# Kernel tuning notes

Measured on AMD Instinct MI355X. Metric: run time of the kernel, lower is better.

## Reference

```python
import jax, jax.numpy as jnp
import numpy as np

N_NODES = 100000
N_EDGES = 1600000
D = 128
NUM_EXPERTS = 8
NUM_LAYERS = 2
EPS = 1e-5


def setup_inputs() -> dict:
    key = jax.random.key(0)
    ks = jax.random.split(key, 8)
    x = jax.random.normal(ks[0], (N_NODES, D), dtype=jnp.float32)
    edge_index = jax.random.randint(ks[1], (2, N_EDGES), 0, N_NODES, dtype=jnp.int64)
    # weights scaled for sane numerics (like torch default inits)
    W_self = jax.random.normal(ks[2], (NUM_EXPERTS, NUM_LAYERS, D, D), dtype=jnp.float32) * 0.05
    W_nbr = jax.random.normal(ks[3], (NUM_EXPERTS, NUM_LAYERS, D, D), dtype=jnp.float32) * 0.05
    b = jax.random.normal(ks[4], (NUM_EXPERTS, NUM_LAYERS, D), dtype=jnp.float32) * 0.05
    gamma = jnp.ones((NUM_EXPERTS, NUM_LAYERS - 1, D), dtype=jnp.float32)
    beta = jnp.zeros((NUM_EXPERTS, NUM_LAYERS - 1, D), dtype=jnp.float32)
    return {"x": x, "edge_index": edge_index, "W_self": W_self, "W_nbr": W_nbr,
            "b": b, "gamma": gamma, "beta": beta}


def _sage_encoder(x, src, dst, inv_deg, W_self, W_nbr, b, gamma, beta):
    # One GraphSAGE-style encoder: per layer, mean-aggregate neighbor feats,
    # transform self + neighbor, then BatchNorm + ReLU (all but last layer).
    h = x
    for l in range(NUM_LAYERS):
        agg = jax.ops.segment_sum(h[src], dst, num_segments=N_NODES) * inv_deg  # [N, d]
        h = h @ W_self[l] + agg @ W_nbr[l] + b[l]
        if l < NUM_LAYERS - 1:
            mean = jnp.mean(h, axis=0)
            var = jnp.var(h, axis=0)
            h = gamma[l] * (h - mean) * jax.lax.rsqrt(var + EPS) + beta[l]
            h = jax.nn.relu(h)
        # dropout: identity in inference mode
    return h  # [N, d]


def reference(x, edge_index, W_self, W_nbr, b, gamma, beta):
    src, dst = edge_index[0], edge_index[1]
    deg = jax.ops.segment_sum(jnp.ones((N_EDGES,), x.dtype), dst, num_segments=N_NODES)
    inv_deg = (1.0 / jnp.maximum(deg, 1.0))[:, None]  # [N, 1]
    outs = [
        _sage_encoder(x, src, dst, inv_deg, W_self[e], W_nbr[e], b[e], gamma[e], beta[e])
        for e in range(NUM_EXPERTS)
    ]
    return jnp.stack(outs, axis=-1)  # [N, hidden, num_experts]
```

## Files before the change

### kernel.cpp

```cpp
#include <hip/hip_runtime.h>
#include <stdint.h>

#define NN 100000
#define NED 1600000
#define DD 128
#define NE 8
#define ND ((size_t)NN * (size_t)DD)
#define NDE (ND * NE)
#define BNEPS 1e-5f

typedef __attribute__((ext_vector_type(8))) short short8;
typedef __attribute__((ext_vector_type(4))) float float4v;
typedef __attribute__((ext_vector_type(4))) unsigned int uint4v;

__device__ __forceinline__ float bf2f(uint32_t h) {
    union { uint32_t u; float f; } c; c.u = h << 16; return c.f;
}
__device__ __forceinline__ uint16_t f2bf(float x) {
    union { float f; uint32_t u; } c; c.f = x;
    uint32_t r = (c.u + 0x7fffu + ((c.u >> 16) & 1u)) >> 16;
    return (uint16_t)r;
}

__global__ __launch_bounds__(256) void k_deg(const int* __restrict__ dst, int* __restrict__ deg) {
    int i = blockIdx.x * 256 + threadIdx.x;
    int stride = gridDim.x * 256;
    for (; i < NED; i += stride) atomicAdd(&deg[dst[i]], 1);
}

__global__ __launch_bounds__(1024) void k_scan1(const int* __restrict__ deg, int* __restrict__ rp,
                                                int* __restrict__ bsum) {
    __shared__ int sh[1024];
    int t = threadIdx.x;
    int i = blockIdx.x * 1024 + t;
    int v = (i < NN) ? deg[i] : 0;
    sh[t] = v; __syncthreads();
    for (int off = 1; off < 1024; off <<= 1) {
        int add = (t >= off) ? sh[t - off] : 0;
        __syncthreads();
        sh[t] += add;
        __syncthreads();
    }
    if (i < NN) rp[i] = sh[t] - v;
    if (t == 1023) bsum[blockIdx.x] = sh[1023];
}

__global__ void k_scan2(int* bsum) {
    if (threadIdx.x == 0) {
        int acc = 0;
        for (int j = 0; j < 98; ++j) { int t = bsum[j]; bsum[j] = acc; acc += t; }
    }
}

__global__ __launch_bounds__(1024) void k_scan3(const int* __restrict__ deg, int* __restrict__ rp,
                                                const int* __restrict__ bsum, int* __restrict__ cur,
                                                float* __restrict__ invd) {
    int i = blockIdx.x * 1024 + threadIdx.x;
    if (i == 0) rp[NN] = NED;
    if (i < NN) {
        int r = rp[i] + bsum[blockIdx.x];
        rp[i] = r; cur[i] = r;
        invd[i] = 1.0f / fmaxf((float)deg[i], 1.0f);
    }
}

__global__ __launch_bounds__(256) void k_scatter(const int* __restrict__ src, const int* __restrict__ dst,
                                                 int* __restrict__ cur, int* __restrict__ esrc) {
    int i = blockIdx.x * 256 + threadIdx.x;
    int stride = gridDim.x * 256;
    for (; i < NED; i += stride) {
        int d = dst[i];
        int p = atomicAdd(&cur[d], 1);
        esrc[p] = src[i];
    }
}

__global__ __launch_bounds__(256) void k_castx(const float* __restrict__ x, uint16_t* __restrict__ xb) {
    size_t i = ((size_t)blockIdx.x * 256 + threadIdx.x) * 8;
    if (i >= ND) return;
    float4 a = *(const float4*)(x + i);
    float4 b = *(const float4*)(x + i + 4);
    uint4 u;
    u.x = (uint32_t)f2bf(a.x) | ((uint32_t)f2bf(a.y) << 16);
    u.y = (uint32_t)f2bf(a.z) | ((uint32_t)f2bf(a.w) << 16);
    u.z = (uint32_t)f2bf(b.x) | ((uint32_t)f2bf(b.y) << 16);
    u.w = (uint32_t)f2bf(b.z) | ((uint32_t)f2bf(b.w) << 16);
    *(uint4*)(xb + i) = u;
}

__global__ __launch_bounds__(256) void k_agg(const uint16_t* __restrict__ sp, uint16_t* __restrict__ dp,
                                             const int* __restrict__ rp, const int* __restrict__ esrc,
                                             const float* __restrict__ invd) {
    int wave = threadIdx.x >> 6, lane = threadIdx.x & 63;
    int node = blockIdx.x * 4 + wave;
    if (node >= NN) return;
    int beg = rp[node], end = rp[node + 1];
    float s0 = 0, s1 = 0, t0 = 0, t1 = 0;
    int i = beg;
    for (; i + 1 < end; i += 2) {
        int a = esrc[i], b = esrc[i + 1];
        uint32_t va = *(const uint32_t*)(sp + (size_t)a * DD + lane * 2);
        uint32_t vb = *(const uint32_t*)(sp + (size_t)b * DD + lane * 2);
        s0 += bf2f(va & 0xffff); s1 += bf2f(va >> 16);
        t0 += bf2f(vb & 0xffff); t1 += bf2f(vb >> 16);
    }
    if (i < end) {
        uint32_t va = *(const uint32_t*)(sp + (size_t)esrc[i] * DD + lane * 2);
        s0 += bf2f(va & 0xffff); s1 += bf2f(va >> 16);
    }
    float id = invd[node];
    s0 = (s0 + t0) * id; s1 = (s1 + t1) * id;
    *(uint32_t*)(dp + (size_t)node * DD + lane * 2) = (uint32_t)f2bf(s0) | ((uint32_t)f2bf(s1) << 16);
}

__device__ __forceinline__ void acc_u4(float* a, uint4 u) {
    a[0] += bf2f(u.x & 0xffffu); a[1] += bf2f(u.x >> 16);
    a[2] += bf2f(u.y & 0xffffu); a[3] += bf2f(u.y >> 16);
    a[4] += bf2f(u.z & 0xffffu); a[5] += bf2f(u.z >> 16);
    a[6] += bf2f(u.w & 0xffffu); a[7] += bf2f(u.w >> 16);
}

__global__ __launch_bounds__(256) void k_agg8(const uint16_t* __restrict__ Hi,
                                              uint16_t* __restrict__ A2i,
                                              const int* __restrict__ rp,
                                              const int* __restrict__ esrc,
                                              const float* __restrict__ invd) {
    int wave = threadIdx.x >> 6, lane = threadIdx.x & 63;
    int node = blockIdx.x * 4 + wave;
    if (node >= NN) return;
    int beg = rp[node], end = rp[node + 1];
    float acc[16];
#pragma unroll
    for (int j = 0; j < 16; ++j) acc[j] = 0.f;
    const size_t loff = (size_t)(lane * 16);
    int i = beg;
    for (; i + 1 < end; i += 2) {
        const uint16_t* pa = Hi + (size_t)esrc[i] * 1024 + loff;
        const uint16_t* pb = Hi + (size_t)esrc[i + 1] * 1024 + loff;
        uint4 a0 = *(const uint4*)pa;
        uint4 a1 = *(const uint4*)(pa + 8);
        uint4 b0 = *(const uint4*)pb;
        uint4 b1 = *(const uint4*)(pb + 8);
        acc_u4(acc, a0); acc_u4(acc + 8, a1);
        acc_u4(acc, b0); acc_u4(acc + 8, b1);
    }
    if (i < end) {
        const uint16_t* pa = Hi + (size_t)esrc[i] * 1024 + loff;
        uint4 a0 = *(const uint4*)pa;
        uint4 a1 = *(const uint4*)(pa + 8);
        acc_u4(acc, a0); acc_u4(acc + 8, a1);
    }
    float id = invd[node];
    uint32_t pk[8];
#pragma unroll
    for (int j = 0; j < 8; ++j)
        pk[j] = (uint32_t)f2bf(acc[2 * j] * id) | ((uint32_t)f2bf(acc[2 * j + 1] * id) << 16);
    uint4v o0 = {pk[0], pk[1], pk[2], pk[3]};
    uint4v o1 = {pk[4], pk[5], pk[6], pk[7]};
    uint16_t* dp = A2i + (size_t)node * 1024 + loff;
    __builtin_nontemporal_store(o0, (uint4v*)dp);
    __builtin_nontemporal_store(o1, (uint4v*)(dp + 8));
}

__global__ __launch_bounds__(256, 2) void k_gemm(
    const float* __restrict__ Wself, const float* __restrict__ Wnbr, const float* __restrict__ bglob,
    int layer,
    const uint16_t* __restrict__ A1, const uint16_t* __restrict__ A2, int a_rstride, int a_ezoff,
    uint16_t* __restrict__ outb, int out_mode, float* __restrict__ outf) {
    __shared__ __align__(16) uint16_t wlds[128 * 256];
    int tid = threadIdx.x;
    int e = blockIdx.z;
    size_t wbase = ((size_t)e * 2 + layer) * (128 * 128);

    for (int i = tid; i < 128 * 32; i += 256) {
        int n = i & 127, g = i >> 7;
        uint16_t tmp[8];
#pragma unroll
        for (int j = 0; j < 8; ++j) {
            int k = g * 8 + j;
            float w = (k < 128) ? Wself[wbase + (size_t)k * 128 + n]
                                : Wnbr[wbase + (size_t)(k - 128) * 128 + n];
            tmp[j] = f2bf(w);
        }
        uint4 u;
        u.x = (uint32_t)tmp[0] | ((uint32_t)tmp[1] << 16);
        u.y = (uint32_t)tmp[2] | ((uint32_t)tmp[3] << 16);
        u.z = (uint32_t)tmp[4] | ((uint32_t)tmp[5] << 16);
        u.w = (uint32_t)tmp[6] | ((uint32_t)tmp[7] << 16);
        *(uint4*)&wlds[n * 256 + (((g ^ n) & 31) << 3)] = u;
    }
    __syncthreads();

    const uint16_t* A1p = A1 + (size_t)e * a_ezoff;
    const uint16_t* A2p = A2 + (size_t)e * a_ezoff;

    int wave = tid >> 6, lane = tid & 63;
    int m = lane & 15, quad = lane >> 4;
    int rowBase = blockIdx.x * 256 + wave * 64;

    float4v acc[4][8];
#pragma unroll
    for (int rt = 0; rt < 4; ++rt)
#pragma unroll
        for (int nt = 0; nt < 8; ++nt)
            acc[rt][nt] = (float4v){0.f, 0.f, 0.f, 0.f};

#pragma unroll
    for (int ks = 0; ks < 8; ++ks) {
        int kk = ks * 32 + quad * 8;
        short8 af[4];
#pragma unroll
        for (int rt = 0; rt < 4; ++rt) {
            int row = rowBase + rt * 16 + m;
            row = row < NN ? row : NN - 1;
            const uint16_t* ap = (kk < 128) ? (A1p + (size_t)row * a_rstride + kk)
                                            : (A2p + (size_t)row * a_rstride + (kk - 128));
            af[rt] = *(const short8*)ap;
        }
        int g = kk >> 3;
#pragma unroll
        for (int nt = 0; nt < 8; ++nt) {
            int n = nt * 16 + m;
            short8 bf = *(const short8*)&wlds[n * 256 + (((g ^ n) & 31) << 3)];
#pragma unroll
            for (int rt = 0; rt < 4; ++rt)
                acc[rt][nt] = __builtin_amdgcn_mfma_f32_16x16x32_bf16(af[rt], bf, acc[rt][nt], 0, 0, 0);
        }
    }

    size_t bofs = ((size_t)e * 2 + layer) * 128;
#pragma unroll
    for (int rt = 0; rt < 4; ++rt) {
#pragma unroll
        for (int nt = 0; nt < 8; ++nt) {
            int col = nt * 16 + m;
            float bv = bglob[bofs + col];
#pragma unroll
            for (int r = 0; r < 4; ++r) {
                int row = rowBase + rt * 16 + quad * 4 + r;
                if (row < NN) {
                    float v = acc[rt][nt][r] + bv;
                    if (out_mode == 0) outb[(size_t)row * 1024 + (size_t)e * 128 + col] = f2bf(v);
                    else if (out_mode == 1) outb[(size_t)e * ND + (size_t)row * DD + col] = f2bf(v);
                    else outf[(size_t)row * 1024 + col * 8 + e] = v;
                }
            }
        }
    }
}

__global__ __launch_bounds__(256) void k_stats(const uint16_t* __restrict__ H, float* __restrict__ stats) {
    int e = blockIdx.y;
    const uint16_t* Hp = H + e * 128;
    int f = threadIdx.x & 127, half = threadIdx.x >> 7;
    float s = 0, ss = 0;
    for (int row = blockIdx.x * 2 + half; row < NN; row += gridDim.x * 2) {
        float v = bf2f(Hp[(size_t)row * 1024 + f]);
        s += v; ss += v * v;
    }
    __shared__ float sh[512];
    sh[threadIdx.x] = s; sh[256 + threadIdx.x] = ss;
    __syncthreads();
    if (half == 0) {
        atomicAdd(&stats[e * 256 + f], sh[f] + sh[128 + f]);
        atomicAdd(&stats[e * 256 + 128 + f], sh[256 + f] + sh[256 + 128 + f]);
    }
}

__global__ void k_coef(const float* __restrict__ stats, const float* __restrict__ gamma,
                       const float* __restrict__ beta, float* __restrict__ coef) {
    int e = blockIdx.x;
    int f = threadIdx.x;
    float s = stats[e * 256 + f], ss = stats[e * 256 + 128 + f];
    float mean = s / (float)NN;
    float var = ss / (float)NN - mean * mean;
    float sc = gamma[e * 128 + f] * rsqrtf(var + BNEPS);
    coef[e * 256 + f] = sc;
    coef[e * 256 + 128 + f] = beta[e * 128 + f] - mean * sc;
}

__global__ __launch_bounds__(256) void k_affine(uint16_t* __restrict__ H, const float* __restrict__ coef) {
    size_t i = ((size_t)blockIdx.x * 256 + threadIdx.x) * 8;
    if (i >= NDE) return;
    int e = (int)((i >> 7) & 7);
    int ff = (int)(i & 127);
    const float* sc = coef + e * 256;
    const float* sf = sc + 128;
    uint4 u = *(const uint4*)(H + i);
    uint32_t w[4] = {u.x, u.y, u.z, u.w};
    uint32_t o[4];
#pragma unroll
    for (int j = 0; j < 4; ++j) {
        float v0 = fmaxf(bf2f(w[j] & 0xffffu) * sc[ff + 2 * j] + sf[ff + 2 * j], 0.f);
        float v1 = fmaxf(bf2f(w[j] >> 16) * sc[ff + 2 * j + 1] + sf[ff + 2 * j + 1], 0.f);
        o[j] = (uint32_t)f2bf(v0) | ((uint32_t)f2bf(v1) << 16);
    }
    uint4 ou = {o[0], o[1], o[2], o[3]};
    *(uint4*)(H + i) = ou;
}

__global__ __launch_bounds__(256) void k_transpose(const uint16_t* __restrict__ O, float* __restrict__ out) {
    size_t t = (size_t)blockIdx.x * 256 + threadIdx.x;
    if (t >= ND / 2) return;
    size_t idx = t * 2;
    float v0[8], v1[8];
#pragma unroll
    for (int e = 0; e < 8; ++e) {
        uint32_t u = *(const uint32_t*)(O + (size_t)e * ND + idx);
        v0[e] = bf2f(u & 0xffff); v1[e] = bf2f(u >> 16);
    }
    float* op = out + idx * 8;
    float4 a = {v0[0], v0[1], v0[2], v0[3]}, b = {v0[4], v0[5], v0[6], v0[7]};
    float4 c = {v1[0], v1[1], v1[2], v1[3]}, d = {v1[4], v1[5], v1[6], v1[7]};
    *(float4*)(op) = a; *(float4*)(op + 4) = b; *(float4*)(op + 8) = c; *(float4*)(op + 12) = d;
}

extern "C" void kernel_launch(void* const* d_in, const int* in_sizes, int n_in,
                              void* d_out, int out_size, void* d_ws, size_t ws_size,
                              hipStream_t stream) {
    const float* x = (const float*)d_in[0];
    const int* ei = (const int*)d_in[1];
    const float* Wself = (const float*)d_in[2];
    const float* Wnbr = (const float*)d_in[3];
    const float* bias = (const float*)d_in[4];
    const float* gamma = (const float*)d_in[5];
    const float* beta = (const float*)d_in[6];
    float* out = (float*)d_out;
    const int* src = ei;
    const int* dst = ei + NED;

    char* ws = (char*)d_ws;
    size_t off = 0;
    auto alloc = [&](size_t b) { size_t p = off; off += (b + 255) & ~(size_t)255; return p; };
    int* deg = (int*)(ws + alloc((size_t)NN * 4));
    int* rp = (int*)(ws + alloc((size_t)(NN + 1) * 4));
    int* cur = (int*)(ws + alloc((size_t)NN * 4));
    int* esrc = (int*)(ws + alloc((size_t)NED * 4));
    float* invd = (float*)(ws + alloc((size_t)NN * 4));
    int* bsum = (int*)(ws + alloc(98 * 4));
    float* stats = (float*)(ws + alloc(NE * 256 * 4));
    float* coef = (float*)(ws + alloc(NE * 256 * 4));
    uint16_t* xb = (uint16_t*)(ws + alloc(ND * 2));
    uint16_t* agg0 = (uint16_t*)(ws + alloc(ND * 2));

    size_t rem = (ws_size > off) ? ws_size - off : 0;
    size_t plane = ND * 2;
    bool useO = rem >= 24 * plane + 4096;

    uint16_t* Hi = (uint16_t*)(ws + alloc(NE * plane));
    uint16_t* A2i = (uint16_t*)(ws + alloc(NE * plane));
    uint16_t* Otmp = useO ? (uint16_t*)(ws + alloc((size_t)NE * plane)) : nullptr;

    hipMemsetAsync(deg, 0, (size_t)NN * 4, stream);
    hipMemsetAsync(stats, 0, NE * 256 * 4, stream);

    k_deg<<<2048, 256, 0, stream>>>(dst, deg);
    k_scan1<<<98, 1024, 0, stream>>>(deg, rp, bsum);
    k_scan2<<<1, 64, 0, stream>>>(bsum);
    k_scan3<<<98, 1024, 0, stream>>>(deg, rp, bsum, cur, invd);
    k_scatter<<<2048, 256, 0, stream>>>(src, dst, cur, esrc);
    k_castx<<<6250, 256, 0, stream>>>(x, xb);

    k_agg<<<25000, 256, 0, stream>>>(xb, agg0, rp, esrc, invd);

    k_gemm<<<dim3(391, 1, NE), 256, 0, stream>>>(Wself, Wnbr, bias, 0,
                                                 xb, agg0, 128, 0, Hi, 0, nullptr);
    k_stats<<<dim3(500, NE), 256, 0, stream>>>(Hi, stats);
    k_coef<<<NE, 128, 0, stream>>>(stats, gamma, beta, coef);
    k_affine<<<50000, 256, 0, stream>>>(Hi, coef);

    k_agg8<<<25000, 256, 0, stream>>>(Hi, A2i, rp, esrc, invd);

    if (useO) {
        k_gemm<<<dim3(391, 1, NE), 256, 0, stream>>>(Wself, Wnbr, bias, 1,
                                                     Hi, A2i, 1024, 128, Otmp, 1, nullptr);
        k_transpose<<<25000, 256, 0, stream>>>(Otmp, out);
    } else {
        k_gemm<<<dim3(391, 1, NE), 256, 0, stream>>>(Wself, Wnbr, bias, 1,
                                                     Hi, A2i, 1024, 128, nullptr, 2, out);
    }
}
```

Before: 1.973 ms.

## Fuse BatchNorm statistics into layer-0 GEMM epilogue and unroll aggregation loops

Computes per-feature sum and sum-of-squares inside the GEMM epilogue. Values are reduced with wave shuffles, then LDS atomics, then global atomics, which removes the separate k_stats pass over the layer-0 activations. The edge-gather loops in both aggregation kernels are unrolled to four neighbors per iteration to keep more loads in flight. Stats are now taken from fp32 values before bf16 rounding. The extra epilogue work and LDS use may add register pressure to the GEMM.

```diff
diff --git a/kernel.cpp b/kernel.cpp
--- a/kernel.cpp
+++ b/kernel.cpp
@@ -95,21 +95,25 @@
     int node = blockIdx.x * 4 + wave;
     if (node >= NN) return;
     int beg = rp[node], end = rp[node + 1];
-    float s0 = 0, s1 = 0, t0 = 0, t1 = 0;
+    float s0 = 0, s1 = 0, t0 = 0, t1 = 0, u0 = 0, u1 = 0, w0 = 0, w1 = 0;
     int i = beg;
-    for (; i + 1 < end; i += 2) {
-        int a = esrc[i], b = esrc[i + 1];
+    for (; i + 3 < end; i += 4) {
+        int a = esrc[i], b = esrc[i + 1], c = esrc[i + 2], d = esrc[i + 3];
         uint32_t va = *(const uint32_t*)(sp + (size_t)a * DD + lane * 2);
         uint32_t vb = *(const uint32_t*)(sp + (size_t)b * DD + lane * 2);
+        uint32_t vc = *(const uint32_t*)(sp + (size_t)c * DD + lane * 2);
+        uint32_t vd = *(const uint32_t*)(sp + (size_t)d * DD + lane * 2);
         s0 += bf2f(va & 0xffff); s1 += bf2f(va >> 16);
         t0 += bf2f(vb & 0xffff); t1 += bf2f(vb >> 16);
-    }
-    if (i < end) {
+        u0 += bf2f(vc & 0xffff); u1 += bf2f(vc >> 16);
+        w0 += bf2f(vd & 0xffff); w1 += bf2f(vd >> 16);
+    }
+    for (; i < end; ++i) {
         uint32_t va = *(const uint32_t*)(sp + (size_t)esrc[i] * DD + lane * 2);
         s0 += bf2f(va & 0xffff); s1 += bf2f(va >> 16);
     }
     float id = invd[node];
-    s0 = (s0 + t0) * id; s1 = (s1 + t1) * id;
+    s0 = (s0 + t0 + u0 + w0) * id; s1 = (s1 + t1 + u1 + w1) * id;
     *(uint32_t*)(dp + (size_t)node * DD + lane * 2) = (uint32_t)f2bf(s0) | ((uint32_t)f2bf(s1) << 16);
 }
 
@@ -134,17 +138,25 @@
     for (int j = 0; j < 16; ++j) acc[j] = 0.f;
     const size_t loff = (size_t)(lane * 16);
     int i = beg;
-    for (; i + 1 < end; i += 2) {
-        const uint16_t* pa = Hi + (size_t)esrc[i] * 1024 + loff;
-        const uint16_t* pb = Hi + (size_t)esrc[i + 1] * 1024 + loff;
-        uint4 a0 = *(const uint4*)pa;
-        uint4 a1 = *(const uint4*)(pa + 8);
-        uint4 b0 = *(const uint4*)pb;
-        uint4 b1 = *(const uint4*)(pb + 8);
+    for (; i + 3 < end; i += 4) {
+        const uint16_t* p0 = Hi + (size_t)esrc[i] * 1024 + loff;
+        const uint16_t* p1 = Hi + (size_t)esrc[i + 1] * 1024 + loff;
+        const uint16_t* p2 = Hi + (size_t)esrc[i + 2] * 1024 + loff;
+        const uint16_t* p3 = Hi + (size_t)esrc[i + 3] * 1024 + loff;
+        uint4 a0 = *(const uint4*)p0;
+        uint4 a1 = *(const uint4*)(p0 + 8);
+        uint4 b0 = *(const uint4*)p1;
+        uint4 b1 = *(const uint4*)(p1 + 8);
+        uint4 c0 = *(const uint4*)p2;
+        uint4 c1 = *(const uint4*)(p2 + 8);
+        uint4 d0 = *(const uint4*)p3;
+        uint4 d1 = *(const uint4*)(p3 + 8);
         acc_u4(acc, a0); acc_u4(acc + 8, a1);
         acc_u4(acc, b0); acc_u4(acc + 8, b1);
-    }
-    if (i < end) {
+        acc_u4(acc, c0); acc_u4(acc + 8, c1);
+        acc_u4(acc, d0); acc_u4(acc + 8, d1);
+    }
+    for (; i < end; ++i) {
         const uint16_t* pa = Hi + (size_t)esrc[i] * 1024 + loff;
         uint4 a0 = *(const uint4*)pa;
         uint4 a1 = *(const uint4*)(pa + 8);
@@ -166,8 +178,11 @@
     const float* __restrict__ Wself, const float* __restrict__ Wnbr, const float* __restrict__ bglob,
     int layer,
     const uint16_t* __restrict__ A1, const uint16_t* __restrict__ A2, int a_rstride, int a_ezoff,
-    uint16_t* __restrict__ outb, int out_mode, float* __restrict__ outf) {
+    uint16_t* __restrict__ outb, int out_mode, float* __restrict__ outf,
+    int do_stats, float* __restrict__ stats) {
     __shared__ __align__(16) uint16_t wlds[128 * 256];
+    __shared__ float ssum[128];
+    __shared__ float ssq[128];
     int tid = threadIdx.x;
     int e = blockIdx.z;
     size_t wbase = ((size_t)e * 2 + layer) * (128 * 128);
@@ -189,6 +204,7 @@
         u.w = (uint32_t)tmp[6] | ((uint32_t)tmp[7] << 16);
         *(uint4*)&wlds[n * 256 + (((g ^ n) & 31) << 3)] = u;
     }
+    if (tid < 128) { ssum[tid] = 0.f; ssq[tid] = 0.f; }
     __syncthreads();
 
     const uint16_t* A1p = A1 + (size_t)e * a_ezoff;
@@ -227,6 +243,10 @@
                 acc[rt][nt] = __builtin_amdgcn_mfma_f32_16x16x32_bf16(af[rt], bf, acc[rt][nt], 0, 0, 0);
         }
     }
+
+    float csum[8], csq[8];
+#pragma unroll
+    for (int nt = 0; nt < 8; ++nt) { csum[nt] = 0.f; csq[nt] = 0.f; }
 
     size_t bofs = ((size_t)e * 2 + layer) * 128;
 #pragma unroll
@@ -243,27 +263,28 @@
                     if (out_mode == 0) outb[(size_t)row * 1024 + (size_t)e * 128 + col] = f2bf(v);
                     else if (out_mode == 1) outb[(size_t)e * ND + (size_t)row * DD + col] = f2bf(v);
                     else outf[(size_t)row * 1024 + col * 8 + e] = v;
+                    if (do_stats) { csum[nt] += v; csq[nt] += v * v; }
                 }
             }
         }
     }
-}
-
-__global__ __launch_bounds__(256) void k_stats(const uint16_t* __restrict__ H, float* __restrict__ stats) {
-    int e = blockIdx.y;
-    const uint16_t* Hp = H + e * 128;
-    int f = threadIdx.x & 127, half = threadIdx.x >> 7;
-    float s = 0, ss = 0;
-    for (int row = blockIdx.x * 2 + half; row < NN; row += gridDim.x * 2) {
-        float v = bf2f(Hp[(size_t)row * 1024 + f]);
-        s += v; ss += v * v;
-    }
-    __shared__ float sh[512];
-    sh[threadIdx.x] = s; sh[256 + threadIdx.x] = ss;
-    __syncthreads();
-    if (half == 0) {
-        atomicAdd(&stats[e * 256 + f], sh[f] + sh[128 + f]);
-        atomicAdd(&stats[e * 256 + 128 + f], sh[256 + f] + sh[256 + 128 + f]);
+
+    if (do_stats) {
+#pragma unroll
+        for (int nt = 0; nt < 8; ++nt) {
+            float s = csum[nt], q = csq[nt];
+            s += __shfl_xor(s, 16); q += __shfl_xor(q, 16);
+            s += __shfl_xor(s, 32); q += __shfl_xor(q, 32);
+            if (quad == 0) {
+                atomicAdd(&ssum[nt * 16 + m], s);
+                atomicAdd(&ssq[nt * 16 + m], q);
+            }
+        }
+        __syncthreads();
+        if (tid < 128) {
+            atomicAdd(&stats[e * 256 + tid], ssum[tid]);
+            atomicAdd(&stats[e * 256 + 128 + tid], ssq[tid]);
+        }
     }
 }
 
@@ -364,8 +385,7 @@
     k_agg<<<25000, 256, 0, stream>>>(xb, agg0, rp, esrc, invd);
 
     k_gemm<<<dim3(391, 1, NE), 256, 0, stream>>>(Wself, Wnbr, bias, 0,
-                                                 xb, agg0, 128, 0, Hi, 0, nullptr);
-    k_stats<<<dim3(500, NE), 256, 0, stream>>>(Hi, stats);
+                                                 xb, agg0, 128, 0, Hi, 0, nullptr, 1, stats);
     k_coef<<<NE, 128, 0, stream>>>(stats, gamma, beta, coef);
     k_affine<<<50000, 256, 0, stream>>>(Hi, coef);
 
@@ -373,10 +393,10 @@
 
     if (useO) {
         k_gemm<<<dim3(391, 1, NE), 256, 0, stream>>>(Wself, Wnbr, bias, 1,
-                                                     Hi, A2i, 1024, 128, Otmp, 1, nullptr);
+                                                     Hi, A2i, 1024, 128, Otmp, 1, nullptr, 0, nullptr);
         k_transpose<<<25000, 256, 0, stream>>>(Otmp, out);
     } else {
         k_gemm<<<dim3(391, 1, NE), 256, 0, stream>>>(Wself, Wnbr, bias, 1,
-                                                     Hi, A2i, 1024, 128, nullptr, 2, out);
-    }
-}
+                                                     Hi, A2i, 1024, 128, nullptr, 2, out, 0, nullptr);
+    }
+}
```

Measured after the change: 1.928 ms. 1.02x faster.
